# Optimization experiments

Hardware: AMD Instinct MI355X
Metric: run time of the kernel (lower is better)

Reference implementation:

```python
import jax, jax.numpy as jnp
import numpy as np

TOP_K = 8      # num_activated_experts
ALPHA = 0.01   # aux_loss_alpha (training mode, seq_aux=False)


def setup_inputs() -> dict:
    key = jax.random.key(0)
    k1, k2 = jax.random.split(key)
    B, S, D, E = 2, 8192, 4096, 64
    hidden_states = jax.random.normal(k1, (B, S, D), dtype=jnp.float32)
    # nn.Parameter(torch.randn(E, D) / sqrt(D))
    weight = jax.random.normal(k2, (E, D), dtype=jnp.float32) / np.float32(np.sqrt(D))
    return {"hidden_states": hidden_states, "weight": weight}


def reference(hidden_states, weight):
    B, S, D = hidden_states.shape
    E = weight.shape[0]
    x = hidden_states.reshape(-1, D)                      # [N, D], N = B*S tokens
    logits = jnp.einsum('nd,ed->ne', x, weight)           # F.linear, no bias
    scores = jax.nn.softmax(logits, axis=-1)              # [N, E]
    topk_weight, topk_idx = jax.lax.top_k(scores, TOP_K)  # [N, K] (torch uses sorted=False; same set)
    # top_k > 1 and norm_topk_prob=False -> no renormalization
    # aux loss (training, seq_aux=False): ce = mean one-hot load, pi = mean scores
    flat_idx = topk_idx.reshape(-1)                       # [N*K]
    ce = jnp.zeros((E,), scores.dtype).at[flat_idx].add(1.0) / flat_idx.size
    pi = scores.mean(axis=0)                              # [E]
    aux_loss = jnp.sum(pi * ce * E) * jnp.asarray(ALPHA, scores.dtype)
    return topk_idx, topk_weight, aux_loss
```

## Files before the change

### kernel.cpp

```cpp
#include <hip/hip_runtime.h>
#include <math.h>

#define DDIM 4096
#define NEXP 64

typedef short s16x8 __attribute__((ext_vector_type(8)));
typedef float f32x4 __attribute__((ext_vector_type(4)));

__device__ __forceinline__ unsigned cvt_pk_bf16(float a, float b) {
  unsigned r;
  asm("v_cvt_pk_bf16_f32 %0, %1, %2" : "=v"(r) : "v"(a), "v"(b));
  return r;
}

__device__ __forceinline__ void split2(float a, float b, unsigned& H,
                                       unsigned& M, unsigned& L) {
  H = cvt_pk_bf16(a, b);
  float h0 = __uint_as_float(H << 16);
  float h1 = __uint_as_float(H & 0xffff0000u);
  float r0 = a - h0, r1 = b - h1;
  M = cvt_pk_bf16(r0, r1);
  float m0 = __uint_as_float(M << 16);
  float m1 = __uint_as_float(M & 0xffff0000u);
  L = cvt_pk_bf16(r0 - m0, r1 - m1);
}

union U8 { unsigned u[4]; s16x8 v; };
__device__ __forceinline__ s16x8 pack8(const unsigned* a) {
  U8 t;
  t.u[0] = a[0]; t.u[1] = a[1]; t.u[2] = a[2]; t.u[3] = a[3];
  return t.v;
}

#define MFMA(A, B, C) __builtin_amdgcn_mfma_f32_16x16x32_bf16(A, B, C, 0, 0, 0)

__global__ __launch_bounds__(1024) void moe_gate_main(
    const float* __restrict__ x,
    const ushort* __restrict__ wf,
    float* __restrict__ out,
    float* __restrict__ pi_g, float* __restrict__ ce_g, int N) {
  __shared__ float smem[17536];
  float* lt = smem;
  float* inv_s = smem + 17408;
  float* ce_lds = smem + 17472;

  const int tid = threadIdx.x;
  const int lane = tid & 63;
  const int wv = tid >> 6;
  const int g = wv >> 2;
  const int sw = wv & 3;
  const int tok0 = blockIdx.x << 6;
  const int rot = ((blockIdx.x * 9) + (g << 3)) & 31;

  const float* xr = x + (size_t)(tok0 + (sw << 4) + (lane & 15)) * DDIM +
                    (g << 10) + ((lane >> 4) << 3);
  const ushort* wfg = wf + (size_t)g * 32 * 12 * 512;

  f32x4 accH[4], accC[4];
#pragma unroll
  for (int eg = 0; eg < 4; ++eg) {
#pragma unroll
    for (int r = 0; r < 4; ++r) { accH[eg][r] = 0.f; accC[eg][r] = 0.f; }
  }

  const int p1 = (rot + 1) & 31, p2 = (rot + 2) & 31, p3 = (rot + 3) & 31;
  float4 x0a = ((const float4*)(xr + rot * 32))[0];
  float4 x0b = ((const float4*)(xr + rot * 32))[1];
  float4 x1a = ((const float4*)(xr + p1 * 32))[0];
  float4 x1b = ((const float4*)(xr + p1 * 32))[1];
  float4 x2a = ((const float4*)(xr + p2 * 32))[0];
  float4 x2b = ((const float4*)(xr + p2 * 32))[1];
  float4 x3a = ((const float4*)(xr + p3 * 32))[0];
  float4 x3b = ((const float4*)(xr + p3 * 32))[1];

#define KSTEP(XA, XB, I)                                                       \
  {                                                                            \
    const int kb = ((I) + rot) & 31;                                           \
    unsigned AH[4], AM[4], AL[4];                                              \
    split2(XA.x, XA.y, AH[0], AM[0], AL[0]);                                   \
    split2(XA.z, XA.w, AH[1], AM[1], AL[1]);                                   \
    split2(XB.x, XB.y, AH[2], AM[2], AL[2]);                                   \
    split2(XB.z, XB.w, AH[3], AM[3], AL[3]);                                   \
    const s16x8 ah = pack8(AH), am = pack8(AM), al = pack8(AL);                \
    {                                                                          \
      const int kn = ((I) + 4 + rot) & 31;                                     \
      XA = ((const float4*)(xr + kn * 32))[0];                                 \
      XB = ((const float4*)(xr + kn * 32))[1];                                 \
    }                                                                          \
    const ushort* wk = wfg + (size_t)kb * (12 * 512) + lane * 8;               \
    _Pragma("unroll") for (int eg = 0; eg < 4; ++eg) {                         \
      const s16x8 bh = *(const s16x8*)(wk + (eg * 3 + 0) * 512);               \
      const s16x8 bm = *(const s16x8*)(wk + (eg * 3 + 1) * 512);               \
      const s16x8 bl = *(const s16x8*)(wk + (eg * 3 + 2) * 512);               \
      accH[eg] = MFMA(ah, bh, accH[eg]);                                       \
      accC[eg] = MFMA(ah, bm, accC[eg]);                                       \
      accC[eg] = MFMA(am, bh, accC[eg]);                                       \
      accC[eg] = MFMA(am, bm, accC[eg]);                                       \
      accC[eg] = MFMA(ah, bl, accC[eg]);                                       \
      accC[eg] = MFMA(al, bh, accC[eg]);                                       \
    }                                                                          \
  }

#pragma unroll 1
  for (int i = 0; i < 32; i += 4) {
    KSTEP(x0a, x0b, i);
    KSTEP(x1a, x1b, i + 1);
    KSTEP(x2a, x2b, i + 2);
    KSTEP(x3a, x3b, i + 3);
  }

  {
    float* ltp = smem + g * 4352;
#pragma unroll
    for (int eg = 0; eg < 4; ++eg) {
#pragma unroll
      for (int r = 0; r < 4; ++r) {
        ltp[(eg * 16 + (lane & 15)) * 68 + (sw << 4) + ((lane >> 4) << 2) + r] =
            accH[eg][r] + accC[eg][r];
      }
    }
  }
  __syncthreads();

  for (int idx = tid; idx < 4352; idx += 1024)
    lt[idx] = (lt[idx] + smem[4352 + idx] + smem[8704 + idx] + smem[13056 + idx]) * 0.015625f;
  __syncthreads();

  if (tid < 64) {
    const int t = tid;
    ce_lds[t] = 0.f;
    float m = -1e30f;
#pragma unroll 1
    for (int e = 0; e < 64; ++e) m = fmaxf(m, lt[e * 68 + t]);
    float ssum = 0.f;
#pragma unroll 1
    for (int e = 0; e < 64; ++e) {
      float p = expf(lt[e * 68 + t] - m);
      lt[e * 68 + t] = p;
      ssum += p;
    }
    inv_s[t] = 1.f / ssum;
  }
  __syncthreads();

  if (tid < 64) {
    const int e = tid;
    float ssum = 0.f;
#pragma unroll 1
    for (int t = 0; t < 64; ++t) ssum += lt[e * 68 + t] * inv_s[t];
    atomicAdd(pi_g + e, ssum);
  }
  __syncthreads();

  if (tid < 64) {
    const int t = tid;
    const float invv = inv_s[t];
    const size_t tg2 = (size_t)(tok0 + t);
#pragma unroll 1
    for (int r = 0; r < 8; ++r) {
      float bv = -1.f;
      int bi = 0;
#pragma unroll 1
      for (int e = 0; e < 64; ++e) {
        float p = lt[e * 68 + t];
        if (p > bv) { bv = p; bi = e; }
      }
      lt[bi * 68 + t] = -1.f;
      atomicAdd(ce_lds + bi, 1.f);
      out[tg2 * 8 + r] = (float)bi;
      out[(size_t)N * 8 + tg2 * 8 + r] = bv * invv;
    }
  }
  __syncthreads();
  if (tid < 64) atomicAdd(ce_g + tid, ce_lds[tid]);
}

__global__ void build_wfrag(const float* __restrict__ w, ushort* __restrict__ wf) {
  const int kb = blockIdx.x;
  const int t = threadIdx.x;
  const int eg = t >> 6, lane = t & 63;
  const int e = (eg << 4) + (lane & 15);
  const int k0 = (kb << 5) + ((lane >> 4) << 3);
  const float* src = w + (size_t)e * DDIM + k0;
  unsigned H[4], M[4], L[4];
#pragma unroll
  for (int i = 0; i < 4; ++i) {
    float a = src[2 * i] * 64.f, b = src[2 * i + 1] * 64.f;
    split2(a, b, H[i], M[i], L[i]);
  }
  const size_t base = ((size_t)kb * 12 + eg * 3) * 512 + (size_t)lane * 8;
  *(uint4*)(wf + base) = make_uint4(H[0], H[1], H[2], H[3]);
  *(uint4*)(wf + base + 512) = make_uint4(M[0], M[1], M[2], M[3]);
  *(uint4*)(wf + base + 1024) = make_uint4(L[0], L[1], L[2], L[3]);
}

__global__ void aux_final(const float* __restrict__ pi_g,
                          const float* __restrict__ ce_g,
                          float* __restrict__ out_aux, int N) {
  const int e = threadIdx.x;
  float v = (pi_g[e] / (float)N) * (ce_g[e] / ((float)N * 8.0f)) * 64.0f * 0.01f;
#pragma unroll
  for (int off = 32; off; off >>= 1) v += __shfl_down(v, off, 64);
  if (e == 0) *out_aux = v;
}

extern "C" void kernel_launch(void* const* d_in, const int* in_sizes, int n_in,
                              void* d_out, int out_size, void* d_ws, size_t ws_size,
                              hipStream_t stream) {
  (void)n_in; (void)out_size; (void)ws_size;
  const float* x = (const float*)d_in[0];
  const float* w = (const float*)d_in[1];
  float* out = (float*)d_out;
  const int N = in_sizes[0] / DDIM;

  ushort* wf = (ushort*)d_ws;
  float* pi_g = (float*)((char*)d_ws + (size_t)128 * 12 * 512 * 2);
  float* ce_g = pi_g + 64;

  hipMemsetAsync(pi_g, 0, 128 * sizeof(float), stream);
  build_wfrag<<<128, 256, 0, stream>>>(w, wf);
  moe_gate_main<<<N / 64, 1024, 0, stream>>>(x, wf, out, pi_g, ce_g, N);
  aux_final<<<1, 64, 0, stream>>>(pi_g, ce_g, out + (size_t)N * 16, N);
}
```

Measured before the change: 143.5 us.

## Double-buffer weight fragments in registers and use nontemporal x loads

Weight fragments are now loaded into two register half-buffers (even/odd expert groups), so the next k-block's first half is prefetched while the current MFMAs run. The x prefetch distance drops from 4 to 2 k-steps, which frees registers for the weight buffers, and the x loads become nontemporal so the streamed activations do not displace cached weights. The intent is to hide weight-load latency behind MFMA work. In exchange, the shorter x prefetch distance gives less latency hiding for the bandwidth-bound x stream.

```diff
diff --git a/kernel.cpp b/kernel.cpp
--- a/kernel.cpp
+++ b/kernel.cpp
@@ -6,6 +6,7 @@
 
 typedef short s16x8 __attribute__((ext_vector_type(8)));
 typedef float f32x4 __attribute__((ext_vector_type(4)));
+typedef float f32x4v __attribute__((ext_vector_type(4)));
 
 __device__ __forceinline__ unsigned cvt_pk_bf16(float a, float b) {
   unsigned r;
@@ -34,6 +35,21 @@
 
 #define MFMA(A, B, C) __builtin_amdgcn_mfma_f32_16x16x32_bf16(A, B, C, 0, 0, 0)
 
+#define HALFW(WB, C0, KB)                                                      \
+  {                                                                            \
+    const ushort* wkp = wfg + (size_t)(KB) * (12 * 512) + (C0) * 512 + lane * 8; \
+    _Pragma("unroll") for (int c = 0; c < 6; ++c)                              \
+        WB[c] = *(const s16x8*)(wkp + c * 512);                                \
+  }
+
+#define MEG(EG, WH, WM, WL)                                                    \
+  accH[EG] = MFMA(ah, WH, accH[EG]);                                           \
+  accC[EG] = MFMA(ah, WM, accC[EG]);                                           \
+  accC[EG] = MFMA(am, WH, accC[EG]);                                           \
+  accC[EG] = MFMA(am, WM, accC[EG]);                                           \
+  accC[EG] = MFMA(ah, WL, accC[EG]);                                           \
+  accC[EG] = MFMA(al, WH, accC[EG]);
+
 __global__ __launch_bounds__(1024) void moe_gate_main(
     const float* __restrict__ x,
     const ushort* __restrict__ wf,
@@ -63,50 +79,44 @@
     for (int r = 0; r < 4; ++r) { accH[eg][r] = 0.f; accC[eg][r] = 0.f; }
   }
 
-  const int p1 = (rot + 1) & 31, p2 = (rot + 2) & 31, p3 = (rot + 3) & 31;
-  float4 x0a = ((const float4*)(xr + rot * 32))[0];
-  float4 x0b = ((const float4*)(xr + rot * 32))[1];
-  float4 x1a = ((const float4*)(xr + p1 * 32))[0];
-  float4 x1b = ((const float4*)(xr + p1 * 32))[1];
-  float4 x2a = ((const float4*)(xr + p2 * 32))[0];
-  float4 x2b = ((const float4*)(xr + p2 * 32))[1];
-  float4 x3a = ((const float4*)(xr + p3 * 32))[0];
-  float4 x3b = ((const float4*)(xr + p3 * 32))[1];
+  s16x8 wEvn[6], wOdd[6];
+
+  HALFW(wEvn, 0, rot);
+  const int p1 = (rot + 1) & 31;
+  f32x4v x0a = __builtin_nontemporal_load((const f32x4v*)(xr + rot * 32));
+  f32x4v x0b = __builtin_nontemporal_load((const f32x4v*)(xr + rot * 32) + 1);
+  f32x4v x1a = __builtin_nontemporal_load((const f32x4v*)(xr + p1 * 32));
+  f32x4v x1b = __builtin_nontemporal_load((const f32x4v*)(xr + p1 * 32) + 1);
 
 #define KSTEP(XA, XB, I)                                                       \
   {                                                                            \
-    const int kb = ((I) + rot) & 31;                                           \
+    const int kbc = ((I) + rot) & 31;                                          \
+    HALFW(wOdd, 6, kbc);      \
     unsigned AH[4], AM[4], AL[4];                                              \
-    split2(XA.x, XA.y, AH[0], AM[0], AL[0]);                                   \
-    split2(XA.z, XA.w, AH[1], AM[1], AL[1]);                                   \
-    split2(XB.x, XB.y, AH[2], AM[2], AL[2]);                                   \
-    split2(XB.z, XB.w, AH[3], AM[3], AL[3]);                                   \
+    split2(XA[0], XA[1], AH[0], AM[0], AL[0]);                                 \
+    split2(XA[2], XA[3], AH[1], AM[1], AL[1]);                                 \
+    split2(XB[0], XB[1], AH[2], AM[2], AL[2]);                                 \
+    split2(XB[2], XB[3], AH[3], AM[3], AL[3]);                                 \
     const s16x8 ah = pack8(AH), am = pack8(AM), al = pack8(AL);                \
     {                                                                          \
-      const int kn = ((I) + 4 + rot) & 31;                                     \
-      XA = ((const float4*)(xr + kn * 32))[0];                                 \
-      XB = ((const float4*)(xr + kn * 32))[1];                                 \
+      const int kn = ((I) + 2 + rot) & 31;                \
+      XA = __builtin_nontemporal_load((const f32x4v*)(xr + kn * 32));          \
+      XB = __builtin_nontemporal_load((const f32x4v*)(xr + kn * 32) + 1);      \
     }                                                                          \
-    const ushort* wk = wfg + (size_t)kb * (12 * 512) + lane * 8;               \
-    _Pragma("unroll") for (int eg = 0; eg < 4; ++eg) {                         \
-      const s16x8 bh = *(const s16x8*)(wk + (eg * 3 + 0) * 512);               \
-      const s16x8 bm = *(const s16x8*)(wk + (eg * 3 + 1) * 512);               \
-      const s16x8 bl = *(const s16x8*)(wk + (eg * 3 + 2) * 512);               \
-      accH[eg] = MFMA(ah, bh, accH[eg]);                                       \
-      accC[eg] = MFMA(ah, bm, accC[eg]);                                       \
-      accC[eg] = MFMA(am, bh, accC[eg]);                                       \
-      accC[eg] = MFMA(am, bm, accC[eg]);                                       \
-      accC[eg] = MFMA(ah, bl, accC[eg]);                                       \
-      accC[eg] = MFMA(al, bh, accC[eg]);                                       \
+    MEG(0, wEvn[0], wEvn[1], wEvn[2]);                                         \
+    MEG(1, wEvn[3], wEvn[4], wEvn[5]);                                         \
+    {                                                                          \
+      const int kbn = ((I) + 1 + rot) & 31;                                    \
+      HALFW(wEvn, 0, kbn);                               \
     }                                                                          \
-  }
-
-#pragma unroll 1
-  for (int i = 0; i < 32; i += 4) {
+    MEG(2, wOdd[0], wOdd[1], wOdd[2]);                                         \
+    MEG(3, wOdd[3], wOdd[4], wOdd[5]);                                         \
+  }
+
+#pragma unroll 1
+  for (int i = 0; i < 32; i += 2) {
     KSTEP(x0a, x0b, i);
     KSTEP(x1a, x1b, i + 1);
-    KSTEP(x2a, x2b, i + 2);
-    KSTEP(x3a, x3b, i + 3);
   }
 
   {
```

New measurement: 165.0 us. 1.15x slower.
